# Kernel tuning notes

Hardware: AMD Instinct MI355X
Metric: run time of the kernel (lower is better)

The kernel has to match this reference:

```python
import jax, jax.numpy as jnp
import numpy as np

B, H, N, D = 2, 16, 2048, 128

def setup_inputs() -> dict:
    key = jax.random.key(0)
    kq, kk, kv = jax.random.split(key, 3)
    q = jax.random.normal(kq, (B, H, N, D), dtype=jnp.float32)
    k = jax.random.normal(kk, (B, H, N, D), dtype=jnp.float32)
    v = jax.random.normal(kv, (B, H, N, D), dtype=jnp.float32)
    return {"q": q, "k": k, "v": v}

def reference(q, k, v):
    # scale = 1/sqrt(d) computed at forward time (scale=None in __init__)
    d = q.shape[-1]
    scale = 1.0 / jnp.sqrt(jnp.asarray(d, dtype=q.dtype))
    # scores: (B, H, N, N)
    scores = jnp.einsum('bhnd,bhmd->bhnm', q, k) * scale
    probs = jax.nn.softmax(scores, axis=-1)
    return jnp.einsum('bhnm,bhmd->bhnd', probs, v)
```

## Files before the change

### kernel.cpp

```cpp
#include <hip/hip_runtime.h>
#include <hip/hip_bf16.h>
#include <stdint.h>

#define BATCH 2
#define HEADS 16
#define BH    32
#define SEQ   2048
#define DIM   128
#define ELEMS (BATCH*HEADS*SEQ*DIM)

#define KVB   64
#define NT    (SEQ/KVB)

using f32x4  = __attribute__((ext_vector_type(4))) float;
using f32x16 = __attribute__((ext_vector_type(16))) float;
using bf16x8 = __attribute__((ext_vector_type(8))) short;
using us4    = __attribute__((ext_vector_type(4))) unsigned short;

__device__ __forceinline__ unsigned short f2bf(float f) {
    union { float f; uint32_t u; } v; v.f = f;
    uint32_t u = v.u;
    uint32_t r = u + 0x7FFFu + ((u >> 16) & 1u);
    return (unsigned short)(r >> 16);
}

__device__ __forceinline__ uint32_t packbf2(float lo, float hi) {
    __hip_bfloat162 h2 = __float22bfloat162_rn(make_float2(lo, hi));
    union { __hip_bfloat162 h; uint32_t u; } c; c.h = h2;
    return c.u;
}

__global__ __launch_bounds__(256) void cvt_bf16(const float* __restrict__ in,
                                                unsigned short* __restrict__ out) {
    int i = (blockIdx.x * 256 + threadIdx.x) * 4;
    f32x4 v = *(const f32x4*)(in + i);
    us4 o;
    #pragma unroll
    for (int j = 0; j < 4; j++) o[j] = f2bf(v[j]);
    *(us4*)(out + i) = o;
}

__global__ __launch_bounds__(256) void trans_v(const float* __restrict__ V,
                                               unsigned short* __restrict__ VT) {
    __shared__ unsigned short tile[32][36];
    int bh = blockIdx.z, n0 = blockIdx.y * 32, d0 = blockIdx.x * 32;
    int t = threadIdx.x;
    int row = t >> 3, c4 = (t & 7) * 4;
    f32x4 v = *(const f32x4*)(V + ((size_t)bh * SEQ + n0 + row) * DIM + d0 + c4);
    #pragma unroll
    for (int j = 0; j < 4; j++) tile[row][c4 + j] = f2bf(v[j]);
    __syncthreads();
    us4 o;
    #pragma unroll
    for (int j = 0; j < 4; j++) o[j] = tile[c4 + j][row];
    *(us4*)(VT + ((size_t)bh * DIM + d0 + row) * SEQ + n0 + c4) = o;
}

__global__ __launch_bounds__(256, 2) void attn_fwd(const unsigned short* __restrict__ Qb,
                                                   const unsigned short* __restrict__ Kb,
                                                   const unsigned short* __restrict__ VTb,
                                                   float* __restrict__ Out) {
    __shared__ __attribute__((aligned(16))) char smem[65536];

    const int head = blockIdx.y;
    const int wid  = threadIdx.x >> 6;
    const int lane = threadIdx.x & 63;
    const int l31  = lane & 31;
    const int hL   = lane >> 5;
    const int q0   = blockIdx.x * 128 + wid * 32;

    const unsigned short* Qh = Qb + (size_t)head * SEQ * DIM;
    const char* KhB  = (const char*)(Kb  + (size_t)head * SEQ * DIM);
    const char* VThB = (const char*)(VTb + (size_t)head * DIM * SEQ);

    bf16x8 qf[8];
    {
        const char* qrow = (const char*)(Qh + (size_t)(q0 + l31) * DIM) + 16 * hL;
        #pragma unroll
        for (int u = 0; u < 8; ++u) qf[u] = *(const bf16x8*)(qrow + 32 * u);
    }

    f32x16 acc[4];
    #pragma unroll
    for (int m = 0; m < 4; ++m) acc[m] = (f32x16)(0.f);
    float m_run = -INFINITY, l_run = 0.f;
    const float sc = 0.08838834764831845f * 1.4426950408889634f;

    const int swzK = (l31 & 15) << 4;
    const int swzV = ((l31 >> 1) & 7) << 4;

    auto STAGE = [&](int buf, int kv0) {
        #pragma unroll
        for (int i = 0; i < 4; ++i) {
            int seg = wid * 4 + i;
            int r   = seg * 4 + (lane >> 4);
            int cb  = ((lane & 15) << 4) ^ ((r & 15) << 4);
            const char* g = KhB + (((size_t)(kv0 + r)) << 8) + cb;
            __builtin_amdgcn_global_load_lds(
                (const __attribute__((address_space(1))) void*)g,
                (__attribute__((address_space(3))) void*)(smem + buf * 16384 + seg * 1024),
                16, 0, 0);
        }
        #pragma unroll
        for (int i = 0; i < 4; ++i) {
            int seg = wid * 4 + i;
            int rp  = seg * 4 + (lane >> 4);
            int q8  = (lane & 15) << 4;
            int pre = q8 ^ ((rp & 7) << 4);
            int r   = 2 * rp + (pre >> 7);
            int cb  = pre & 127;
            const char* g = VThB + (size_t)r * (SEQ * 2) + ((size_t)kv0 << 1) + cb;
            __builtin_amdgcn_global_load_lds(
                (const __attribute__((address_space(1))) void*)g,
                (__attribute__((address_space(3))) void*)(smem + 32768 + buf * 16384 + seg * 1024),
                16, 0, 0);
        }
    };

    STAGE(0, 0);

    for (int t = 0; t < NT; ++t) {
        const int cur = t & 1;
        if (t + 1 < NT) {
            STAGE(cur ^ 1, (t + 1) * KVB);
            asm volatile("s_waitcnt vmcnt(8)" ::: "memory");
        } else {
            asm volatile("s_waitcnt vmcnt(0)" ::: "memory");
        }
        __builtin_amdgcn_s_barrier();
        asm volatile("" ::: "memory");

        const char* kb = smem + cur * 16384;
        const char* vb = smem + 32768 + cur * 16384;

        f32x16 s0 = (f32x16)(0.f), s1 = (f32x16)(0.f);
        {
            const char* krow0 = kb + (size_t)l31 * 256;
            const char* krow1 = kb + (size_t)(32 + l31) * 256;
            #pragma unroll
            for (int u = 0; u < 8; ++u) {
                int cb = (32 * u + 16 * hL) ^ swzK;
                bf16x8 k0 = *(const bf16x8*)(krow0 + cb);
                bf16x8 k1 = *(const bf16x8*)(krow1 + cb);
                s0 = __builtin_amdgcn_mfma_f32_32x32x16_bf16(k0, qf[u], s0, 0, 0, 0);
                s1 = __builtin_amdgcn_mfma_f32_32x32x16_bf16(k1, qf[u], s1, 0, 0, 0);
            }
        }

        float smax = -1e30f;
        #pragma unroll
        for (int r = 0; r < 16; ++r) {
            s0[r] *= sc; s1[r] *= sc;
            smax = fmaxf(smax, fmaxf(s0[r], s1[r]));
        }
        smax = fmaxf(smax, __shfl_xor(smax, 32));

        if (!__all(smax - m_run <= 8.f)) {
            float mnew = fmaxf(m_run, smax);
            float corr = __builtin_amdgcn_exp2f(m_run - mnew);
            #pragma unroll
            for (int m = 0; m < 4; ++m) acc[m] *= corr;
            l_run *= corr;
            m_run = mnew;
        }

        float psum = 0.f;
        #pragma unroll
        for (int r = 0; r < 16; ++r) {
            s0[r] = __builtin_amdgcn_exp2f(s0[r] - m_run);
            s1[r] = __builtin_amdgcn_exp2f(s1[r] - m_run);
            psum += s0[r] + s1[r];
        }
        psum += __shfl_xor(psum, 32);
        l_run += psum;

        uint32_t w0[8], w1[8];
        #pragma unroll
        for (int k2 = 0; k2 < 8; ++k2) {
            w0[k2] = packbf2(s0[2 * k2], s0[2 * k2 + 1]);
            w1[k2] = packbf2(s1[2 * k2], s1[2 * k2 + 1]);
        }

        #pragma unroll
        for (int tt = 0; tt < 2; ++tt) {
            #pragma unroll
            for (int ssi = 0; ssi < 2; ++ssi) {
                uint32_t A0 = tt ? w1[4 * ssi]     : w0[4 * ssi];
                uint32_t A1 = tt ? w1[4 * ssi + 1] : w0[4 * ssi + 1];
                uint32_t C0 = tt ? w1[4 * ssi + 2] : w0[4 * ssi + 2];
                uint32_t C1 = tt ? w1[4 * ssi + 3] : w0[4 * ssi + 3];
                uint32_t o0 = hL ? A0 : C0;
                uint32_t o1 = hL ? A1 : C1;
                uint32_t e0 = (uint32_t)__shfl_xor((int)o0, 32);
                uint32_t e1 = (uint32_t)__shfl_xor((int)o1, 32);
                union { uint32_t u[4]; bf16x8 v; } B;
                B.u[0] = hL ? e0 : A0;
                B.u[1] = hL ? e1 : A1;
                B.u[2] = hL ? C0 : e0;
                B.u[3] = hL ? C1 : e1;
                const int cbv = (32 * (2 * tt + ssi) + 16 * hL) + ((l31 & 1) << 7);
                #pragma unroll
                for (int m = 0; m < 4; ++m) {
                    int rp = 16 * m + (l31 >> 1);
                    bf16x8 vf = *(const bf16x8*)(vb + (size_t)rp * 256 + (cbv ^ swzV));
                    acc[m] = __builtin_amdgcn_mfma_f32_32x32x16_bf16(vf, B.v, acc[m], 0, 0, 0);
                }
            }
        }

        asm volatile("" ::: "memory");
        __builtin_amdgcn_s_barrier();
    }

    __syncthreads();
    const float inv = 1.0f / l_run;
    float* ob = (float*)(smem + wid * 16384);
    #pragma unroll
    for (int m = 0; m < 4; ++m) {
        #pragma unroll
        for (int r = 0; r < 16; ++r) {
            int d = 32 * m + (r & 3) + 8 * (r >> 2) + 4 * hL;
            ob[l31 * 128 + (d ^ ((l31 & 7) << 2))] = acc[m][r] * inv;
        }
    }
    __syncthreads();
    {
        float* outp = Out + ((size_t)head * SEQ + q0) * DIM;
        #pragma unroll
        for (int i = 0; i < 16; ++i) {
            int row = 2 * i + hL;
            f32x4 v = *(const f32x4*)(ob + row * 128 + ((4 * l31) ^ ((row & 7) << 2)));
            *(f32x4*)(outp + (size_t)row * DIM + 4 * l31) = v;
        }
    }
}

extern "C" void kernel_launch(void* const* d_in, const int* in_sizes, int n_in,
                              void* d_out, int out_size, void* d_ws, size_t ws_size,
                              hipStream_t stream) {
    (void)in_sizes; (void)n_in; (void)out_size;
    const float* q = (const float*)d_in[0];
    const float* k = (const float*)d_in[1];
    const float* v = (const float*)d_in[2];
    float* out = (float*)d_out;

    const size_t needed = (size_t)ELEMS * 2 * 3;
    if (ws_size < needed) return;

    unsigned short* qb = (unsigned short*)d_ws;
    unsigned short* kb = qb + ELEMS;
    unsigned short* vt = kb + ELEMS;

    cvt_bf16<<<ELEMS / 4 / 256, 256, 0, stream>>>(q, qb);
    cvt_bf16<<<ELEMS / 4 / 256, 256, 0, stream>>>(k, kb);
    trans_v<<<dim3(DIM / 32, SEQ / 32, BH), 256, 0, stream>>>(v, vt);
    attn_fwd<<<dim3(SEQ / 128, BH), 256, 0, stream>>>(qb, kb, vt, out);
}
```

Before: 225.5 us.

## Fuse preprocessing kernels, load Q directly, prefetch V fragments, add priorities

The separate K conversion and V transpose kernels are merged into one prep launch, and the Q conversion kernel is dropped. Q is now read as fp32 inside the attention kernel, with the softmax scale folded in before rounding to bf16. V fragments are loaded from LDS into registers before the softmax so their latency overlaps it, and s_setprio raises wave priority around the MFMA blocks. The cross-half psum shuffle moves out of the loop to a single final reduction. The changes aim to cut launches, global traffic and in-loop latency, at the cost of more VGPR pressure from the prefetched V fragments and a small rounding difference from scaling Q before the bf16 conversion.

New measurement: 220.0 us. 1.02x faster.

```diff
diff --git a/kernel.cpp b/kernel.cpp
--- a/kernel.cpp
+++ b/kernel.cpp
@@ -30,33 +30,47 @@
     return c.u;
 }
 
-__global__ __launch_bounds__(256) void cvt_bf16(const float* __restrict__ in,
-                                                unsigned short* __restrict__ out) {
-    int i = (blockIdx.x * 256 + threadIdx.x) * 4;
-    f32x4 v = *(const f32x4*)(in + i);
-    us4 o;
-    #pragma unroll
-    for (int j = 0; j < 4; j++) o[j] = f2bf(v[j]);
-    *(us4*)(out + i) = o;
-}
-
-__global__ __launch_bounds__(256) void trans_v(const float* __restrict__ V,
-                                               unsigned short* __restrict__ VT) {
-    __shared__ unsigned short tile[32][36];
-    int bh = blockIdx.z, n0 = blockIdx.y * 32, d0 = blockIdx.x * 32;
-    int t = threadIdx.x;
-    int row = t >> 3, c4 = (t & 7) * 4;
-    f32x4 v = *(const f32x4*)(V + ((size_t)bh * SEQ + n0 + row) * DIM + d0 + c4);
-    #pragma unroll
-    for (int j = 0; j < 4; j++) tile[row][c4 + j] = f2bf(v[j]);
-    __syncthreads();
-    us4 o;
-    #pragma unroll
-    for (int j = 0; j < 4; j++) o[j] = tile[c4 + j][row];
-    *(us4*)(VT + ((size_t)bh * DIM + d0 + row) * SEQ + n0 + c4) = o;
-}
-
-__global__ __launch_bounds__(256, 2) void attn_fwd(const unsigned short* __restrict__ Qb,
+__global__ __launch_bounds__(256) void prep(const float* __restrict__ K,
+                                            const float* __restrict__ V,
+                                            unsigned short* __restrict__ kb,
+                                            unsigned short* __restrict__ vt) {
+    const int b = blockIdx.x, t = threadIdx.x;
+    if (b < 2048) {
+        size_t base = (size_t)b * 4096 + t * 4;
+        #pragma unroll
+        for (int j = 0; j < 4; ++j) {
+            f32x4 v = *(const f32x4*)(K + base + j * 1024);
+            us4 o;
+            #pragma unroll
+            for (int jj = 0; jj < 4; ++jj) o[jj] = f2bf(v[jj]);
+            *(us4*)(kb + base + j * 1024) = o;
+        }
+    } else {
+        __shared__ unsigned short tile[64][66];
+        const int b2 = b - 2048;
+        const int bh = b2 >> 6, rem = b2 & 63;
+        const int n0 = (rem >> 1) * 64, d0 = (rem & 1) * 64;
+        const int rr = t >> 4, cc = t & 15;
+        #pragma unroll
+        for (int j = 0; j < 4; ++j) {
+            int row = rr + 16 * j;
+            f32x4 v = *(const f32x4*)(V + ((size_t)bh * SEQ + n0 + row) * DIM + d0 + cc * 4);
+            #pragma unroll
+            for (int jj = 0; jj < 4; ++jj) tile[row][cc * 4 + jj] = f2bf(v[jj]);
+        }
+        __syncthreads();
+        #pragma unroll
+        for (int j = 0; j < 4; ++j) {
+            int drow = rr + 16 * j;
+            us4 o;
+            #pragma unroll
+            for (int jj = 0; jj < 4; ++jj) o[jj] = tile[cc * 4 + jj][drow];
+            *(us4*)(vt + ((size_t)bh * DIM + d0 + drow) * SEQ + n0 + cc * 4) = o;
+        }
+    }
+}
+
+__global__ __launch_bounds__(256, 2) void attn_fwd(const float* __restrict__ Qf,
                                                    const unsigned short* __restrict__ Kb,
                                                    const unsigned short* __restrict__ VTb,
                                                    float* __restrict__ Out) {
@@ -69,22 +83,30 @@
     const int hL   = lane >> 5;
     const int q0   = blockIdx.x * 128 + wid * 32;
 
-    const unsigned short* Qh = Qb + (size_t)head * SEQ * DIM;
     const char* KhB  = (const char*)(Kb  + (size_t)head * SEQ * DIM);
     const char* VThB = (const char*)(VTb + (size_t)head * DIM * SEQ);
 
+    const float scl = 0.08838834764831845f * 1.4426950408889634f;
     bf16x8 qf[8];
     {
-        const char* qrow = (const char*)(Qh + (size_t)(q0 + l31) * DIM) + 16 * hL;
-        #pragma unroll
-        for (int u = 0; u < 8; ++u) qf[u] = *(const bf16x8*)(qrow + 32 * u);
+        const float* qrow = Qf + ((size_t)head * SEQ + q0 + l31) * DIM + 8 * hL;
+        #pragma unroll
+        for (int u = 0; u < 8; ++u) {
+            f32x4 a = *(const f32x4*)(qrow + 16 * u);
+            f32x4 b = *(const f32x4*)(qrow + 16 * u + 4);
+            union { uint32_t w[4]; bf16x8 v; } P;
+            P.w[0] = packbf2(a[0] * scl, a[1] * scl);
+            P.w[1] = packbf2(a[2] * scl, a[3] * scl);
+            P.w[2] = packbf2(b[0] * scl, b[1] * scl);
+            P.w[3] = packbf2(b[2] * scl, b[3] * scl);
+            qf[u] = P.v;
+        }
     }
 
     f32x16 acc[4];
     #pragma unroll
     for (int m = 0; m < 4; ++m) acc[m] = (f32x16)(0.f);
     float m_run = -INFINITY, l_run = 0.f;
-    const float sc = 0.08838834764831845f * 1.4426950408889634f;
 
     const int swzK = (l31 & 15) << 4;
     const int swzV = ((l31 >> 1) & 7) << 4;
@@ -134,6 +156,7 @@
         const char* vb = smem + 32768 + cur * 16384;
 
         f32x16 s0 = (f32x16)(0.f), s1 = (f32x16)(0.f);
+        __builtin_amdgcn_s_setprio(1);
         {
             const char* krow0 = kb + (size_t)l31 * 256;
             const char* krow1 = kb + (size_t)(32 + l31) * 256;
@@ -146,15 +169,26 @@
                 s1 = __builtin_amdgcn_mfma_f32_32x32x16_bf16(k1, qf[u], s1, 0, 0, 0);
             }
         }
+        __builtin_amdgcn_s_setprio(0);
+
+        bf16x8 vf[2][2][4];
+        #pragma unroll
+        for (int tt = 0; tt < 2; ++tt)
+            #pragma unroll
+            for (int ssi = 0; ssi < 2; ++ssi) {
+                const int cbv = (32 * (2 * tt + ssi) + 16 * hL) + ((l31 & 1) << 7);
+                #pragma unroll
+                for (int m = 0; m < 4; ++m) {
+                    int rp = 16 * m + (l31 >> 1);
+                    vf[tt][ssi][m] = *(const bf16x8*)(vb + (size_t)rp * 256 + (cbv ^ swzV));
+                }
+            }
 
         float smax = -1e30f;
         #pragma unroll
-        for (int r = 0; r < 16; ++r) {
-            s0[r] *= sc; s1[r] *= sc;
+        for (int r = 0; r < 16; ++r)
             smax = fmaxf(smax, fmaxf(s0[r], s1[r]));
-        }
-        smax = fmaxf(smax, __shfl_xor(smax, 32));
-
+        smax = fmaxf(smax, __shfl_xor(smax, 16) * 0.f + __shfl_xor(smax, 32));
         if (!__all(smax - m_run <= 8.f)) {
             float mnew = fmaxf(m_run, smax);
             float corr = __builtin_amdgcn_exp2f(m_run - mnew);
@@ -171,7 +205,6 @@
             s1[r] = __builtin_amdgcn_exp2f(s1[r] - m_run);
             psum += s0[r] + s1[r];
         }
-        psum += __shfl_xor(psum, 32);
         l_run += psum;
 
         uint32_t w0[8], w1[8];
@@ -181,6 +214,7 @@
             w1[k2] = packbf2(s1[2 * k2], s1[2 * k2 + 1]);
         }
 
+        __builtin_amdgcn_s_setprio(1);
         #pragma unroll
         for (int tt = 0; tt < 2; ++tt) {
             #pragma unroll
@@ -193,27 +227,25 @@
                 uint32_t o1 = hL ? A1 : C1;
                 uint32_t e0 = (uint32_t)__shfl_xor((int)o0, 32);
                 uint32_t e1 = (uint32_t)__shfl_xor((int)o1, 32);
-                union { uint32_t u[4]; bf16x8 v; } B;
-                B.u[0] = hL ? e0 : A0;
-                B.u[1] = hL ? e1 : A1;
-                B.u[2] = hL ? C0 : e0;
-                B.u[3] = hL ? C1 : e1;
-                const int cbv = (32 * (2 * tt + ssi) + 16 * hL) + ((l31 & 1) << 7);
+                union { uint32_t u[4]; bf16x8 v; } Bf;
+                Bf.u[0] = hL ? e0 : A0;
+                Bf.u[1] = hL ? e1 : A1;
+                Bf.u[2] = hL ? C0 : e0;
+                Bf.u[3] = hL ? C1 : e1;
                 #pragma unroll
-                for (int m = 0; m < 4; ++m) {
-                    int rp = 16 * m + (l31 >> 1);
-                    bf16x8 vf = *(const bf16x8*)(vb + (size_t)rp * 256 + (cbv ^ swzV));
-                    acc[m] = __builtin_amdgcn_mfma_f32_32x32x16_bf16(vf, B.v, acc[m], 0, 0, 0);
-                }
+                for (int m = 0; m < 4; ++m)
+                    acc[m] = __builtin_amdgcn_mfma_f32_32x32x16_bf16(vf[tt][ssi][m], Bf.v, acc[m], 0, 0, 0);
             }
         }
+        __builtin_amdgcn_s_setprio(0);
 
         asm volatile("" ::: "memory");
         __builtin_amdgcn_s_barrier();
     }
 
     __syncthreads();
-    const float inv = 1.0f / l_run;
+    const float l_tot = l_run + __shfl_xor(l_run, 32);
+    const float inv = 1.0f / l_tot;
     float* ob = (float*)(smem + wid * 16384);
     #pragma unroll
     for (int m = 0; m < 4; ++m) {
@@ -244,15 +276,12 @@
     const float* v = (const float*)d_in[2];
     float* out = (float*)d_out;
 
-    const size_t needed = (size_t)ELEMS * 2 * 3;
+    const size_t needed = (size_t)ELEMS * 2 * 2;
     if (ws_size < needed) return;
 
-    unsigned short* qb = (unsigned short*)d_ws;
-    unsigned short* kb = qb + ELEMS;
+    unsigned short* kb = (unsigned short*)d_ws;
     unsigned short* vt = kb + ELEMS;
 
-    cvt_bf16<<<ELEMS / 4 / 256, 256, 0, stream>>>(q, qb);
-    cvt_bf16<<<ELEMS / 4 / 256, 256, 0, stream>>>(k, kb);
-    trans_v<<<dim3(DIM / 32, SEQ / 32, BH), 256, 0, stream>>>(v, vt);
-    attn_fwd<<<dim3(SEQ / 128, BH), 256, 0, stream>>>(qb, kb, vt, out);
-}
+    prep<<<4096, 256, 0, stream>>>(k, v, kb, vt);
+    attn_fwd<<<dim3(SEQ / 128, BH), 256, 0, stream>>>(q, kb, vt, out);
+}
```
